# Kernel tuning notes

Hardware: AMD Instinct MI355X
Metric: run time of the kernel (lower is better)

Reference implementation:

```python
import jax, jax.numpy as jnp
import numpy as np

N_EXPERTS = 8
TOP_K = 2


def setup_inputs() -> dict:
    key = jax.random.key(0)
    ks = jax.random.split(key, 5)
    B, S, D = 4, 2048, 1024
    H = 2 * D  # SwiGLU hidden = 2 * embeddings_dims
    E = N_EXPERTS
    scale_d = 1.0 / np.sqrt(D)
    scale_h = 1.0 / np.sqrt(H)
    return {
        "x": jax.random.normal(ks[0], (B, S, D), dtype=jnp.float32),
        "Wg": jax.random.normal(ks[1], (D, E), dtype=jnp.float32) * scale_d,
        "W1": jax.random.normal(ks[2], (E, D, H), dtype=jnp.float32) * scale_d,
        "W2": jax.random.normal(ks[3], (E, D, H), dtype=jnp.float32) * scale_d,
        "W3": jax.random.normal(ks[4], (E, H, D), dtype=jnp.float32) * scale_h,
    }


def _swiglu(x, w1, w2, w3):
    # x: [B,S,D]; w1,w2: [D,H]; w3: [H,D]
    a = x @ w1
    swish = a * jax.nn.sigmoid(a)
    return (swish * (x @ w2)) @ w3


def reference(x, Wg, W1, W2, W3):
    # Gating (noisy_topk disabled -> deterministic path)
    gate = x @ Wg                                   # [B,S,E]
    top_vals, top_idx = jax.lax.top_k(gate, TOP_K)  # [B,S,K]
    probs = jax.nn.softmax(top_vals, axis=-1)       # softmax over top-k values

    out = jnp.zeros_like(x)
    for e in range(N_EXPERTS):
        # combine weight for expert e per token (0 if not routed)
        w_e = jnp.sum(jnp.where(top_idx == e, probs, 0.0), axis=-1)  # [B,S]
        out = out + _swiglu(x, W1[e], W2[e], W3[e]) * w_e[..., None]
    return out
```

## Files before the change

### kernel.cpp

```cpp
#include <hip/hip_runtime.h>
#include <stdint.h>
#include <math.h>

#define NTOK  8192
#define DIM   1024
#define HID   2048
#define NE    8

typedef __attribute__((ext_vector_type(8))) short short8;
typedef __attribute__((ext_vector_type(4))) float f32x4;

__device__ __forceinline__ unsigned short f2bf(float f) {
  union { float f; unsigned u; } a; a.f = f;
  unsigned u = a.u;
  u += 0x7fffu + ((u >> 16) & 1u);
  return (unsigned short)(u >> 16);
}

__device__ __forceinline__ float bf2f(unsigned short s) {
  union { unsigned u; float f; } a; a.u = ((unsigned)s) << 16;
  return a.f;
}

__device__ __forceinline__ void gl2lds16(const unsigned short* g, unsigned short* l) {
  __builtin_amdgcn_global_load_lds(
      (const __attribute__((address_space(1))) unsigned int*)g,
      (__attribute__((address_space(3))) unsigned int*)l,
      16, 0, 0);
}

__global__ __launch_bounds__(256) void transpose_all_kernel(
    const float* __restrict__ W1, const float* __restrict__ W2, const float* __restrict__ W3,
    unsigned short* __restrict__ w1t, unsigned short* __restrict__ w2t,
    unsigned short* __restrict__ w3t) {
  __shared__ unsigned short tileT[64][72];
  int b = blockIdx.x;
  int which = b >> 12;
  int rem = b & 4095;
  const float* in;
  unsigned short* out;
  int R, C, bx, by, e;
  if (which < 2) {
    R = DIM; C = HID;
    bx = rem & 31; by = (rem >> 5) & 15; e = rem >> 9;
    in = (which == 0 ? W1 : W2);
    out = (which == 0 ? w1t : w2t);
  } else {
    R = HID; C = DIM;
    bx = rem & 15; by = (rem >> 4) & 31; e = rem >> 9;
    in = W3; out = w3t;
  }
  const float* ine = in + (size_t)e * R * C + (size_t)(by * 64) * C + bx * 64;
  unsigned short* oute = out + (size_t)e * R * C + (size_t)(bx * 64) * R + by * 64;
  int t = threadIdx.x;
  #pragma unroll
  for (int i = 0; i < 4; i++) {
    int idx = t + i * 256;
    int r = idx >> 4, c = (idx & 15) * 4;
    float4 v = *(const float4*)(ine + (size_t)r * C + c);
    tileT[c + 0][r] = f2bf(v.x);
    tileT[c + 1][r] = f2bf(v.y);
    tileT[c + 2][r] = f2bf(v.z);
    tileT[c + 3][r] = f2bf(v.w);
  }
  __syncthreads();
  #pragma unroll
  for (int i = 0; i < 2; i++) {
    int idx = t + i * 256;
    int rr = idx >> 3, cc = (idx & 7) * 8;
    *(uint4*)(oute + (size_t)rr * R + cc) = *(const uint4*)(&tileT[rr][cc]);
  }
}

__global__ __launch_bounds__(256) void gate_kernel(
    const float* __restrict__ x, const float* __restrict__ Wg,
    unsigned short* __restrict__ xb,
    int* __restrict__ eidx, float* __restrict__ eprob, int* __restrict__ cnt) {
  if (blockIdx.x == 0 && threadIdx.x < NE) cnt[threadIdx.x] = 0;
  int wid = threadIdx.x >> 6;
  int lane = threadIdx.x & 63;
  int t = blockIdx.x * 4 + wid;
  const float* xr = x + (size_t)t * DIM;
  unsigned short* xbr = xb + (size_t)t * DIM;
  float acc[NE];
  #pragma unroll
  for (int e = 0; e < NE; e++) acc[e] = 0.f;
  #pragma unroll
  for (int it = 0; it < DIM / 64; it++) {
    int d = it * 64 + lane;
    float xv = xr[d];
    xbr[d] = f2bf(xv);
    const float4* wr = (const float4*)(Wg + d * NE);
    float4 w0 = wr[0], w1 = wr[1];
    acc[0] += xv * w0.x; acc[1] += xv * w0.y; acc[2] += xv * w0.z; acc[3] += xv * w0.w;
    acc[4] += xv * w1.x; acc[5] += xv * w1.y; acc[6] += xv * w1.z; acc[7] += xv * w1.w;
  }
  #pragma unroll
  for (int e = 0; e < NE; e++) {
    float v = acc[e];
    #pragma unroll
    for (int off = 32; off > 0; off >>= 1) v += __shfl_xor(v, off);
    acc[e] = v;
  }
  if (lane == 0) {
    int i0 = 0; float v0 = acc[0];
    #pragma unroll
    for (int e = 1; e < NE; e++) if (acc[e] > v0) { v0 = acc[e]; i0 = e; }
    int i1 = -1; float v1 = -3.4e38f;
    #pragma unroll
    for (int e = 0; e < NE; e++) if (e != i0 && acc[e] > v1) { v1 = acc[e]; i1 = e; }
    float e1 = expf(v1 - v0);
    float p0 = 1.f / (1.f + e1);
    float p1 = e1 / (1.f + e1);
    eidx[t] = i0 | (i1 << 16);
    eprob[2 * t] = p0;
    eprob[2 * t + 1] = p1;
  }
}

__global__ __launch_bounds__(512) void route_kernel(
    const int* __restrict__ eidx,
    int* __restrict__ cnt, int* __restrict__ tok_list, int* __restrict__ slotpos) {
  __shared__ int lhist[NE];
  __shared__ int gbase[NE];
  int tid = threadIdx.x;
  if (tid < NE) lhist[tid] = 0;
  __syncthreads();
  int t = blockIdx.x * 512 + tid;
  int pk = eidx[t];
  int i0 = pk & 0xffff, i1 = pk >> 16;
  int l0 = atomicAdd(&lhist[i0], 1);
  int l1 = atomicAdd(&lhist[i1], 1);
  __syncthreads();
  if (tid < NE) gbase[tid] = atomicAdd(&cnt[tid], lhist[tid]);
  __syncthreads();
  int s0 = gbase[i0] + l0;
  int s1 = gbase[i1] + l1;
  tok_list[i0 * NTOK + s0] = t;
  tok_list[i1 * NTOK + s1] = t;
  slotpos[2 * t] = (i0 << 16) | s0;
  slotpos[2 * t + 1] = (i1 << 16) | s1;
}

__global__ __launch_bounds__(256, 3) void gemm1_kernel(
    const unsigned short* __restrict__ xb,
    const unsigned short* __restrict__ w1t,
    const unsigned short* __restrict__ w2t,
    const int* __restrict__ cnt,
    const int* __restrict__ tok_list,
    unsigned short* __restrict__ hbuf) {
  int e = blockIdx.z;
  int count = cnt[e];
  int mt = blockIdx.y;
  if (mt * 128 >= count) return;
  int nt = blockIdx.x;

  __shared__ __align__(16) unsigned short As[128 * 64];
  __shared__ __align__(16) unsigned short Bs1[64 * 64];
  __shared__ __align__(16) unsigned short Bs2[64 * 64];
  __shared__ int toks[128];

  int tid = threadIdx.x;
  if (tid < 128) {
    int r = mt * 128 + tid;
    toks[tid] = tok_list[e * NTOK + (r < count ? r : 0)];
  }
  __syncthreads();

  int wid = tid >> 6, lane = tid & 63;
  int wm = wid >> 1, wn = wid & 1;
  int m16 = lane & 15, quad = lane >> 4;

  const unsigned short* W1e = w1t + (size_t)e * HID * DIM + (size_t)(nt * 64) * DIM;
  const unsigned short* W2e = w2t + (size_t)e * HID * DIM + (size_t)(nt * 64) * DIM;

  const unsigned short* aptr[4];
  #pragma unroll
  for (int i = 0; i < 4; i++) {
    int slot = wid * 256 + i * 64 + lane;
    int r = slot >> 3, c = slot & 7, g = c ^ (r & 7);
    aptr[i] = xb + (size_t)toks[r] * DIM + g * 8;
  }
  const unsigned short *b1p[2], *b2p[2];
  #pragma unroll
  for (int i = 0; i < 2; i++) {
    int slot = wid * 128 + i * 64 + lane;
    int r = slot >> 3, c = slot & 7, g = c ^ (r & 7);
    b1p[i] = W1e + (size_t)r * DIM + g * 8;
    b2p[i] = W2e + (size_t)r * DIM + g * 8;
  }

  f32x4 acc1[4][2], acc2[4][2];
  f32x4 zz = {0.f, 0.f, 0.f, 0.f};
  #pragma unroll
  for (int i = 0; i < 4; i++)
    #pragma unroll
    for (int j = 0; j < 2; j++) { acc1[i][j] = zz; acc2[i][j] = zz; }

  for (int k0 = 0; k0 < DIM; k0 += 64) {
    #pragma unroll
    for (int i = 0; i < 4; i++)
      gl2lds16(aptr[i] + k0, As + (wid * 256 + i * 64) * 8);
    #pragma unroll
    for (int i = 0; i < 2; i++) {
      gl2lds16(b1p[i] + k0, Bs1 + (wid * 128 + i * 64) * 8);
      gl2lds16(b2p[i] + k0, Bs2 + (wid * 128 + i * 64) * 8);
    }
    __syncthreads();
    #pragma unroll
    for (int ks = 0; ks < 2; ks++) {
      int ga = ks * 4 + quad;
      short8 af[4], b1f[2], b2f[2];
      #pragma unroll
      for (int fm = 0; fm < 4; fm++) {
        int ra = wm * 64 + fm * 16 + m16;
        af[fm] = *(const short8*)(As + ra * 64 + (ga ^ (ra & 7)) * 8);
      }
      #pragma unroll
      for (int fn = 0; fn < 2; fn++) {
        int rb = wn * 32 + fn * 16 + m16;
        b1f[fn] = *(const short8*)(Bs1 + rb * 64 + (ga ^ (rb & 7)) * 8);
        b2f[fn] = *(const short8*)(Bs2 + rb * 64 + (ga ^ (rb & 7)) * 8);
      }
      #pragma unroll
      for (int fm = 0; fm < 4; fm++)
        #pragma unroll
        for (int fn = 0; fn < 2; fn++) {
          acc1[fm][fn] = __builtin_amdgcn_mfma_f32_16x16x32_bf16(af[fm], b1f[fn], acc1[fm][fn], 0, 0, 0);
          acc2[fm][fn] = __builtin_amdgcn_mfma_f32_16x16x32_bf16(af[fm], b2f[fn], acc2[fm][fn], 0, 0, 0);
        }
    }
    __syncthreads();
  }

  int hb = 0;
  #pragma unroll
  for (int j = 0; j < NE; j++) if (j < e) hb += cnt[j];
  #pragma unroll
  for (int fm = 0; fm < 4; fm++)
    #pragma unroll
    for (int fn = 0; fn < 2; fn++)
      #pragma unroll
      for (int r = 0; r < 4; r++) {
        int row = wm * 64 + fm * 16 + quad * 4 + r;
        if (mt * 128 + row < count) {
          float a = acc1[fm][fn][r];
          float v = acc2[fm][fn][r];
          float h = (a / (1.f + __expf(-a))) * v;
          int col = nt * 64 + wn * 32 + fn * 16 + m16;
          hbuf[(size_t)(hb + mt * 128 + row) * HID + col] = f2bf(h);
        }
      }
}

__global__ __launch_bounds__(256, 4) void gemm2_kernel(
    const unsigned short* __restrict__ hbuf,
    const unsigned short* __restrict__ w3t,
    const int* __restrict__ cnt,
    unsigned short* __restrict__ ybuf) {
  int e = blockIdx.z;
  int count = cnt[e];
  int mt = blockIdx.y;
  if (mt * 64 >= count) return;
  int nt = blockIdx.x;
  int hb = 0;
  #pragma unroll
  for (int j = 0; j < NE; j++) if (j < e) hb += cnt[j];

  __shared__ __align__(16) unsigned short As[64 * 64];
  __shared__ __align__(16) unsigned short Bs[128 * 64];

  int tid = threadIdx.x;
  int wid = tid >> 6, lane = tid & 63;
  int m16 = lane & 15, quad = lane >> 4;

  const unsigned short* W3e = w3t + (size_t)e * DIM * HID + (size_t)(nt * 128) * HID;

  const unsigned short *aptr[2], *bptr[4];
  #pragma unroll
  for (int i = 0; i < 2; i++) {
    int slot = tid + 256 * i;
    int r = slot >> 3, c = slot & 7, g = c ^ (r & 7);
    int gr = mt * 64 + r;
    int rc = (gr < count) ? gr : (count - 1);
    aptr[i] = hbuf + (size_t)(hb + rc) * HID + g * 8;
  }
  #pragma unroll
  for (int i = 0; i < 4; i++) {
    int slot = tid + 256 * i;
    int r = slot >> 3, c = slot & 7, g = c ^ (r & 7);
    bptr[i] = W3e + (size_t)r * HID + g * 8;
  }

  f32x4 acc[4][2];
  f32x4 zz = {0.f, 0.f, 0.f, 0.f};
  #pragma unroll
  for (int i = 0; i < 4; i++)
    #pragma unroll
    for (int j = 0; j < 2; j++) acc[i][j] = zz;

  for (int k0 = 0; k0 < HID; k0 += 64) {
    #pragma unroll
    for (int i = 0; i < 2; i++)
      gl2lds16(aptr[i] + k0, As + (tid >> 6) * 0 + ((size_t)(256 * i) + (tid & ~63) + (tid & 63)) * 8);
    #pragma unroll
    for (int i = 0; i < 4; i++)
      gl2lds16(bptr[i] + k0, Bs + ((size_t)(256 * i) + tid) * 8);
    __syncthreads();
    #pragma unroll
    for (int ks = 0; ks < 2; ks++) {
      int ga = ks * 4 + quad;
      short8 af[4], bf[2];
      #pragma unroll
      for (int fm = 0; fm < 4; fm++) {
        int ra = fm * 16 + m16;
        af[fm] = *(const short8*)(As + ra * 64 + (ga ^ (ra & 7)) * 8);
      }
      #pragma unroll
      for (int fn = 0; fn < 2; fn++) {
        int rb = wid * 32 + fn * 16 + m16;
        bf[fn] = *(const short8*)(Bs + rb * 64 + (ga ^ (rb & 7)) * 8);
      }
      #pragma unroll
      for (int fm = 0; fm < 4; fm++)
        #pragma unroll
        for (int fn = 0; fn < 2; fn++)
          acc[fm][fn] = __builtin_amdgcn_mfma_f32_16x16x32_bf16(af[fm], bf[fn], acc[fm][fn], 0, 0, 0);
    }
    __syncthreads();
  }

  #pragma unroll
  for (int fm = 0; fm < 4; fm++)
    #pragma unroll
    for (int fn = 0; fn < 2; fn++)
      #pragma unroll
      for (int r = 0; r < 4; r++) {
        int row = fm * 16 + quad * 4 + r;
        if (mt * 64 + row < count) {
          int col = nt * 128 + wid * 32 + fn * 16 + m16;
          ybuf[(size_t)(hb + mt * 64 + row) * DIM + col] = f2bf(acc[fm][fn][r]);
        }
      }
}

__global__ __launch_bounds__(256) void combine_kernel(
    const unsigned short* __restrict__ ybuf, const int* __restrict__ cnt,
    const int* __restrict__ slotpos, const float* __restrict__ eprob,
    float* __restrict__ out) {
  __shared__ int sbase[NE];
  if (threadIdx.x == 0) {
    int s = 0;
    #pragma unroll
    for (int e = 0; e < NE; e++) { sbase[e] = s; s += cnt[e]; }
  }
  __syncthreads();
  int d = threadIdx.x * 4;
  #pragma unroll
  for (int i = 0; i < 8; i++) {
    int t = blockIdx.x * 8 + i;
    int ps0 = slotpos[2 * t], ps1 = slotpos[2 * t + 1];
    int r0 = sbase[ps0 >> 16] + (ps0 & 0xffff);
    int r1 = sbase[ps1 >> 16] + (ps1 & 0xffff);
    float p0 = eprob[2 * t], p1 = eprob[2 * t + 1];
    ushort4 y0 = *(const ushort4*)(ybuf + (size_t)r0 * DIM + d);
    ushort4 y1 = *(const ushort4*)(ybuf + (size_t)r1 * DIM + d);
    float4 o;
    o.x = p0 * bf2f(y0.x) + p1 * bf2f(y1.x);
    o.y = p0 * bf2f(y0.y) + p1 * bf2f(y1.y);
    o.z = p0 * bf2f(y0.z) + p1 * bf2f(y1.z);
    o.w = p0 * bf2f(y0.w) + p1 * bf2f(y1.w);
    *(float4*)(out + (size_t)t * DIM + d) = o;
  }
}

extern "C" void kernel_launch(void* const* d_in, const int* in_sizes, int n_in,
                              void* d_out, int out_size, void* d_ws, size_t ws_size,
                              hipStream_t stream) {
  const float* x  = (const float*)d_in[0];
  const float* Wg = (const float*)d_in[1];
  const float* W1 = (const float*)d_in[2];
  const float* W2 = (const float*)d_in[3];
  const float* W3 = (const float*)d_in[4];
  float* out = (float*)d_out;

  char* ws = (char*)d_ws;
  size_t off = 0;
  int* cnt = (int*)(ws + off); off += 256;
  int* eidx = (int*)(ws + off); off += (size_t)NTOK * 4;
  float* eprob = (float*)(ws + off); off += (size_t)NTOK * 2 * 4;
  int* slotpos = (int*)(ws + off); off += (size_t)NTOK * 2 * 4;
  int* tok_list = (int*)(ws + off); off += (size_t)NE * NTOK * 4;
  unsigned short* xb  = (unsigned short*)(ws + off); off += (size_t)NTOK * DIM * 2;
  unsigned short* w1t = (unsigned short*)(ws + off); off += (size_t)NE * DIM * HID * 2;
  unsigned short* w2t = (unsigned short*)(ws + off); off += (size_t)NE * DIM * HID * 2;
  unsigned short* w3t = (unsigned short*)(ws + off); off += (size_t)NE * DIM * HID * 2;
  unsigned short* hbuf = (unsigned short*)(ws + off); off += (size_t)NTOK * 2 * HID * 2;
  unsigned short* ybuf = w1t;

  gate_kernel<<<NTOK / 4, 256, 0, stream>>>(x, Wg, xb, eidx, eprob, cnt);
  transpose_all_kernel<<<3 * 4096, 256, 0, stream>>>(W1, W2, W3, w1t, w2t, w3t);
  route_kernel<<<NTOK / 512, 512, 0, stream>>>(eidx, cnt, tok_list, slotpos);
  gemm1_kernel<<<dim3(HID / 64, NTOK / 128, NE), 256, 0, stream>>>(xb, w1t, w2t, cnt, tok_list, hbuf);
  gemm2_kernel<<<dim3(DIM / 128, NTOK / 64, NE), 256, 0, stream>>>(hbuf, w3t, cnt, ybuf);
  combine_kernel<<<NTOK / 8, 256, 0, stream>>>(ybuf, cnt, slotpos, eprob, out);
}
```

Before: 515.0 us.

## Fuse routing into weight transpose and overlap W3 transpose with gemm1

Merges the routing kernel into a prep kernel that also transposes W1/W2, and moves the W3 transpose into extra blocks of the gemm1 launch. This removes two kernel launches and lets the W3 conversion run alongside the expert GEMM blocks. gemm1 switches to a flattened 1D grid with a shared-memory union and a higher occupancy hint (launch bounds 4). The gemm2 LDS destination address now uses the wave base instead of the per-thread address, which matches the per-wave semantics of global_load_lds. Risks include the extra register pressure from the occupancy hint and the cost of the early-exit transpose branch.

```diff
diff --git a/kernel.cpp b/kernel.cpp
--- a/kernel.cpp
+++ b/kernel.cpp
@@ -29,30 +29,9 @@
       16, 0, 0);
 }
 
-__global__ __launch_bounds__(256) void transpose_all_kernel(
-    const float* __restrict__ W1, const float* __restrict__ W2, const float* __restrict__ W3,
-    unsigned short* __restrict__ w1t, unsigned short* __restrict__ w2t,
-    unsigned short* __restrict__ w3t) {
-  __shared__ unsigned short tileT[64][72];
-  int b = blockIdx.x;
-  int which = b >> 12;
-  int rem = b & 4095;
-  const float* in;
-  unsigned short* out;
-  int R, C, bx, by, e;
-  if (which < 2) {
-    R = DIM; C = HID;
-    bx = rem & 31; by = (rem >> 5) & 15; e = rem >> 9;
-    in = (which == 0 ? W1 : W2);
-    out = (which == 0 ? w1t : w2t);
-  } else {
-    R = HID; C = DIM;
-    bx = rem & 15; by = (rem >> 4) & 31; e = rem >> 9;
-    in = W3; out = w3t;
-  }
-  const float* ine = in + (size_t)e * R * C + (size_t)(by * 64) * C + bx * 64;
-  unsigned short* oute = out + (size_t)e * R * C + (size_t)(bx * 64) * R + by * 64;
-  int t = threadIdx.x;
+__device__ __forceinline__ void transpose_tile(
+    const float* __restrict__ ine, unsigned short* __restrict__ oute,
+    int R, int C, unsigned short (*tileT)[72], int t) {
   #pragma unroll
   for (int i = 0; i < 4; i++) {
     int idx = t + i * 256;
@@ -118,49 +97,77 @@
   }
 }
 
-__global__ __launch_bounds__(512) void route_kernel(
+__global__ __launch_bounds__(256) void prep_kernel(
+    const float* __restrict__ W1, const float* __restrict__ W2,
+    unsigned short* __restrict__ w1t, unsigned short* __restrict__ w2t,
     const int* __restrict__ eidx,
     int* __restrict__ cnt, int* __restrict__ tok_list, int* __restrict__ slotpos) {
+  __shared__ unsigned short tileT[64][72];
   __shared__ int lhist[NE];
   __shared__ int gbase[NE];
+  int b = blockIdx.x;
   int tid = threadIdx.x;
-  if (tid < NE) lhist[tid] = 0;
-  __syncthreads();
-  int t = blockIdx.x * 512 + tid;
-  int pk = eidx[t];
-  int i0 = pk & 0xffff, i1 = pk >> 16;
-  int l0 = atomicAdd(&lhist[i0], 1);
-  int l1 = atomicAdd(&lhist[i1], 1);
-  __syncthreads();
-  if (tid < NE) gbase[tid] = atomicAdd(&cnt[tid], lhist[tid]);
-  __syncthreads();
-  int s0 = gbase[i0] + l0;
-  int s1 = gbase[i1] + l1;
-  tok_list[i0 * NTOK + s0] = t;
-  tok_list[i1 * NTOK + s1] = t;
-  slotpos[2 * t] = (i0 << 16) | s0;
-  slotpos[2 * t + 1] = (i1 << 16) | s1;
-}
-
-__global__ __launch_bounds__(256, 3) void gemm1_kernel(
+  if (b < 32) {
+    if (tid < NE) lhist[tid] = 0;
+    __syncthreads();
+    int t = b * 256 + tid;
+    int pk = eidx[t];
+    int i0 = pk & 0xffff, i1 = pk >> 16;
+    int l0 = atomicAdd(&lhist[i0], 1);
+    int l1 = atomicAdd(&lhist[i1], 1);
+    __syncthreads();
+    if (tid < NE) gbase[tid] = atomicAdd(&cnt[tid], lhist[tid]);
+    __syncthreads();
+    int s0 = gbase[i0] + l0;
+    int s1 = gbase[i1] + l1;
+    tok_list[i0 * NTOK + s0] = t;
+    tok_list[i1 * NTOK + s1] = t;
+    slotpos[2 * t] = (i0 << 16) | s0;
+    slotpos[2 * t + 1] = (i1 << 16) | s1;
+    return;
+  }
+  int rem = b - 32;
+  int which = rem >> 12;
+  rem &= 4095;
+  int bx = rem & 31, by = (rem >> 5) & 15, e = rem >> 9;
+  const float* in = which ? W2 : W1;
+  unsigned short* out = which ? w2t : w1t;
+  const float* ine = in + (size_t)e * DIM * HID + (size_t)(by * 64) * HID + bx * 64;
+  unsigned short* oute = out + (size_t)e * DIM * HID + (size_t)(bx * 64) * DIM + by * 64;
+  transpose_tile(ine, oute, DIM, HID, tileT, tid);
+}
+
+__global__ __launch_bounds__(256, 4) void gemm1_kernel(
     const unsigned short* __restrict__ xb,
     const unsigned short* __restrict__ w1t,
     const unsigned short* __restrict__ w2t,
+    const float* __restrict__ W3, unsigned short* __restrict__ w3t,
     const int* __restrict__ cnt,
     const int* __restrict__ tok_list,
     unsigned short* __restrict__ hbuf) {
-  int e = blockIdx.z;
+  __shared__ __align__(16) unsigned char smem[33280];
+  unsigned short* As  = (unsigned short*)smem;
+  unsigned short* Bs1 = (unsigned short*)(smem + 16384);
+  unsigned short* Bs2 = (unsigned short*)(smem + 24576);
+  int* toks = (int*)(smem + 32768);
+
+  int b = blockIdx.x;
+  int tid = threadIdx.x;
+
+  if (b >= 16384) {
+    unsigned short (*tileT)[72] = (unsigned short (*)[72])smem;
+    int rem = b - 16384;
+    int bx = rem & 15, by = (rem >> 4) & 31, e = rem >> 9;
+    const float* ine = W3 + (size_t)e * HID * DIM + (size_t)(by * 64) * DIM + bx * 64;
+    unsigned short* oute = w3t + (size_t)e * HID * DIM + (size_t)(bx * 64) * HID + by * 64;
+    transpose_tile(ine, oute, HID, DIM, tileT, tid);
+    return;
+  }
+
+  int nt = b & 31, mt = (b >> 5) & 63, e = b >> 11;
   int count = cnt[e];
-  int mt = blockIdx.y;
   if (mt * 128 >= count) return;
-  int nt = blockIdx.x;
-
-  __shared__ __align__(16) unsigned short As[128 * 64];
-  __shared__ __align__(16) unsigned short Bs1[64 * 64];
-  __shared__ __align__(16) unsigned short Bs2[64 * 64];
-  __shared__ int toks[128];
-
-  int tid = threadIdx.x;
+
   if (tid < 128) {
     int r = mt * 128 + tid;
     toks[tid] = tok_list[e * NTOK + (r < count ? r : 0)];
@@ -302,10 +309,10 @@
   for (int k0 = 0; k0 < HID; k0 += 64) {
     #pragma unroll
     for (int i = 0; i < 2; i++)
-      gl2lds16(aptr[i] + k0, As + (tid >> 6) * 0 + ((size_t)(256 * i) + (tid & ~63) + (tid & 63)) * 8);
+      gl2lds16(aptr[i] + k0, As + (i * 256 + (tid & ~63)) * 8);
     #pragma unroll
     for (int i = 0; i < 4; i++)
-      gl2lds16(bptr[i] + k0, Bs + ((size_t)(256 * i) + tid) * 8);
+      gl2lds16(bptr[i] + k0, Bs + (i * 256 + (tid & ~63)) * 8);
     __syncthreads();
     #pragma unroll
     for (int ks = 0; ks < 2; ks++) {
@@ -399,9 +406,8 @@
   unsigned short* ybuf = w1t;
 
   gate_kernel<<<NTOK / 4, 256, 0, stream>>>(x, Wg, xb, eidx, eprob, cnt);
-  transpose_all_kernel<<<3 * 4096, 256, 0, stream>>>(W1, W2, W3, w1t, w2t, w3t);
-  route_kernel<<<NTOK / 512, 512, 0, stream>>>(eidx, cnt, tok_list, slotpos);
-  gemm1_kernel<<<dim3(HID / 64, NTOK / 128, NE), 256, 0, stream>>>(xb, w1t, w2t, cnt, tok_list, hbuf);
+  prep_kernel<<<32 + 2 * 4096, 256, 0, stream>>>(W1, W2, w1t, w2t, eidx, cnt, tok_list, slotpos);
+  gemm1_kernel<<<16384 + 4096, 256, 0, stream>>>(xb, w1t, w2t, W3, w3t, cnt, tok_list, hbuf);
   gemm2_kernel<<<dim3(DIM / 128, NTOK / 64, NE), 256, 0, stream>>>(hbuf, w3t, cnt, ybuf);
   combine_kernel<<<NTOK / 8, 256, 0, stream>>>(ybuf, cnt, slotpos, eprob, out);
 }
```

Result: slower. 541.7 us (+5.2%).
